# Kernel optimization log

Hardware: AMD Instinct MI355X
Metric: run time of the kernel (lower is better)

Reference implementation:

```python
import jax, jax.numpy as jnp
import numpy as np

B, S, D, H = 4, 2048, 1024, 16
HD = D // H  # head_dim = 64


def setup_inputs() -> dict:
    key = jax.random.key(0)
    ks = jax.random.split(key, 14)
    s = 0.02
    return {
        "inputs_q": jax.random.normal(ks[0], (B, S, D), jnp.float32),
        "pos_emb_q": jax.random.normal(ks[1], (1, S, D), jnp.float32),
        "pos_emb_k": jax.random.normal(ks[2], (1, S, D), jnp.float32),
        "pos_emb_v": jax.random.normal(ks[3], (1, S, D), jnp.float32),
        "attention_bias": jax.random.normal(ks[4], (1, 1, S, S), jnp.float32),
        "attention_bias_kv": jax.random.normal(ks[5], (B, S), jnp.float32),
        "wq": jax.random.normal(ks[6], (D, H, HD), jnp.float32) * s,
        "bq": jnp.zeros((H, HD), jnp.float32),
        "wk": jax.random.normal(ks[7], (D, H, HD), jnp.float32) * s,
        "bk": jnp.zeros((H, HD), jnp.float32),
        "wv": jax.random.normal(ks[8], (D, H, HD), jnp.float32) * s,
        "bv": jnp.zeros((H, HD), jnp.float32),
        "wo": jax.random.normal(ks[9], (H, HD, D), jnp.float32) * s,
        "bo": jnp.zeros((D,), jnp.float32),
    }


def reference(inputs_q, pos_emb_q, pos_emb_k, pos_emb_v, attention_bias,
              attention_bias_kv, wq, bq, wk, bk, wv, bv, wo, bo):
    # Self-attention: inputs_kv = inputs_q. Additive pos-embs BEFORE projection.
    q_in = inputs_q + pos_emb_q
    k_in = inputs_q + pos_emb_k
    v_in = inputs_q + pos_emb_v
    # QKV DenseGeneral: [B,S,D] -> [B,S,H,HD]
    q = jnp.einsum('bsd,dhk->bshk', q_in, wq) + bq
    k = jnp.einsum('bsd,dhk->bshk', k_in, wk) + bk
    v = jnp.einsum('bsd,dhk->bshk', v_in, wv) + bv
    # Scaled dot-product attention with full bias + key-only bias.
    q = q / jnp.sqrt(jnp.asarray(HD, q.dtype))
    scores = jnp.einsum('bqhk,bshk->bhqs', q, k)  # [B,H,Sq,Sk]
    scores = scores + attention_bias + attention_bias_kv[:, None, None, :]
    attn = jax.nn.softmax(scores, axis=-1)
    x = jnp.einsum('bhqs,bshk->bqhk', attn, v)  # [B,S,H,HD]
    # Output projection contracting (H, HD) -> D.
    out = jnp.einsum('bqhk,hkd->bqd', x, wo) + bo
    return out
```

## Files before the change

### kernel.cpp

```cpp
#include <hip/hip_runtime.h>

typedef __attribute__((ext_vector_type(8))) short short8;
typedef __attribute__((ext_vector_type(4))) float f32x4;

#define MFMA16(a, b, c) __builtin_amdgcn_mfma_f32_16x16x32_bf16(a, b, c, 0, 0, 0)

#define SEQ 2048
#define DIM 1024
#define NH 16
#define HD 64
#define LOG2E 1.4426950408889634f

__device__ __forceinline__ ushort f2bf(float f) {
  union { float f; unsigned u; } v; v.f = f;
  unsigned r = (v.u + 0x7FFFu + ((v.u >> 16) & 1u)) >> 16;
  return (ushort)r;
}

__device__ __forceinline__ ushort bf1(float f) {
  unsigned r;
  asm("v_cvt_pk_bf16_f32 %0, %1, %2" : "=v"(r) : "v"(f), "v"(f));
  return (ushort)(r & 0xffffu);
}

__device__ __forceinline__ float exp2fn(float x) {
#if __has_builtin(__builtin_amdgcn_exp2f)
  return __builtin_amdgcn_exp2f(x);
#else
  return exp2f(x);
#endif
}

__global__ __launch_bounds__(256) void prep_a(
    const float* __restrict__ x, const float* __restrict__ pq,
    const float* __restrict__ pk, const float* __restrict__ pv,
    ushort* __restrict__ aq, ushort* __restrict__ ak, ushort* __restrict__ av) {
  int i = (blockIdx.x * 256 + threadIdx.x) * 4;
  int pi = i & (SEQ * DIM - 1);
  float4 xv = *(const float4*)(x + i);
  float4 q4 = *(const float4*)(pq + pi);
  float4 k4 = *(const float4*)(pk + pi);
  float4 v4 = *(const float4*)(pv + pi);
  ushort4 o;
  o.x = f2bf(xv.x + q4.x); o.y = f2bf(xv.y + q4.y);
  o.z = f2bf(xv.z + q4.z); o.w = f2bf(xv.w + q4.w);
  *(ushort4*)(aq + i) = o;
  o.x = f2bf(xv.x + k4.x); o.y = f2bf(xv.y + k4.y);
  o.z = f2bf(xv.z + k4.z); o.w = f2bf(xv.w + k4.w);
  *(ushort4*)(ak + i) = o;
  o.x = f2bf(xv.x + v4.x); o.y = f2bf(xv.y + v4.y);
  o.z = f2bf(xv.z + v4.z); o.w = f2bf(xv.w + v4.w);
  *(ushort4*)(av + i) = o;
}

__global__ __launch_bounds__(256) void transpose_w(
    const float* __restrict__ src, ushort* __restrict__ dst) {
  __shared__ float t[32][33];
  int tx = threadIdx.x & 31, ty = threadIdx.x >> 5;
  int x0 = blockIdx.x * 32, y0 = blockIdx.y * 32;
#pragma unroll
  for (int j = 0; j < 32; j += 8) t[ty + j][tx] = src[(size_t)(y0 + ty + j) * DIM + x0 + tx];
  __syncthreads();
#pragma unroll
  for (int j = 0; j < 32; j += 8)
    dst[(size_t)(x0 + ty + j) * DIM + y0 + tx] = f2bf(t[tx][ty + j]);
}

template <int MODE>
__global__ __launch_bounds__(256) void gemm128(
    const ushort* __restrict__ A, const ushort* __restrict__ Bt,
    const float* __restrict__ bias, void* __restrict__ outp, float scale) {
  constexpr int K = 1024, LDA = 40;
  __shared__ __align__(16) ushort As[128 * LDA];
  __shared__ __align__(16) ushort Bs[128 * LDA];
  const int tid = threadIdx.x;
  const int wave = tid >> 6, lane = tid & 63;
  const int wr = wave >> 1, wc = wave & 1;
  const int g = lane >> 4, l15 = lane & 15;
  const int bm = blockIdx.x, bn = blockIdx.y;
  const int r0 = tid >> 2, c0 = (tid & 3) * 8;
  const ushort* Ap = A + (size_t)(bm * 128 + r0) * K + c0;
  const ushort* Bp = Bt + (size_t)(bn * 128 + r0) * K + c0;
  f32x4 acc[4][4] = {};

  uint4 ra0 = *(const uint4*)(Ap);
  uint4 ra1 = *(const uint4*)(Ap + (size_t)64 * K);
  uint4 rb0 = *(const uint4*)(Bp);
  uint4 rb1 = *(const uint4*)(Bp + (size_t)64 * K);

  for (int kt = 0; kt < K; kt += 32) {
    __syncthreads();
    *(uint4*)&As[r0 * LDA + c0] = ra0;
    *(uint4*)&As[(r0 + 64) * LDA + c0] = ra1;
    *(uint4*)&Bs[r0 * LDA + c0] = rb0;
    *(uint4*)&Bs[(r0 + 64) * LDA + c0] = rb1;
    __syncthreads();
    if (kt + 32 < K) {
      ra0 = *(const uint4*)(Ap + kt + 32);
      ra1 = *(const uint4*)(Ap + (size_t)64 * K + kt + 32);
      rb0 = *(const uint4*)(Bp + kt + 32);
      rb1 = *(const uint4*)(Bp + (size_t)64 * K + kt + 32);
    }
    short8 af[4], bfr[4];
#pragma unroll
    for (int m = 0; m < 4; ++m)
      af[m] = *(const short8*)&As[(wr * 64 + m * 16 + l15) * LDA + g * 8];
#pragma unroll
    for (int n = 0; n < 4; ++n)
      bfr[n] = *(const short8*)&Bs[(wc * 64 + n * 16 + l15) * LDA + g * 8];
#pragma unroll
    for (int m = 0; m < 4; ++m)
#pragma unroll
      for (int n = 0; n < 4; ++n) acc[m][n] = MFMA16(af[m], bfr[n], acc[m][n]);
  }

#pragma unroll
  for (int m = 0; m < 4; ++m) {
    int row = bm * 128 + wr * 64 + m * 16 + g * 4;
#pragma unroll
    for (int n = 0; n < 4; ++n) {
      int col = bn * 128 + wc * 64 + n * 16 + l15;
      float bv = bias[col];
#pragma unroll
      for (int j = 0; j < 4; ++j) {
        float v = (acc[m][n][j] + bv) * scale;
        int r = row + j;
        if (MODE == 0) {
          int b = r >> 11, s = r & (SEQ - 1), h = col >> 6, hd = col & (HD - 1);
          ((ushort*)outp)[((size_t)((b * NH + h) * SEQ + s)) * HD + hd] = f2bf(v);
        } else if (MODE == 2) {
          int b = r >> 11, s = r & (SEQ - 1), h = col >> 6, hd = col & (HD - 1);
          ((ushort*)outp)[((size_t)((b * NH + h) * HD + hd)) * SEQ + s] = f2bf(v);
        } else {
          ((float*)outp)[(size_t)r * DIM + col] = v;
        }
      }
    }
  }
}

__global__ __launch_bounds__(256) void attn5(
    const ushort* __restrict__ Q, const ushort* __restrict__ K,
    const ushort* __restrict__ VT, const float* __restrict__ abias,
    const float* __restrict__ kvbias, ushort* __restrict__ X) {
  constexpr int LDK = 72, LDV = 72, LDP = 72;
  __shared__ __align__(16) ushort Ks[64 * LDK];
  __shared__ __align__(16) ushort Vs[64 * LDV];
  __shared__ __align__(16) ushort Ps[4][32 * LDP];
  const int tid = threadIdx.x;
  const int w = tid >> 6, lane = tid & 63, g = lane >> 4, l15 = lane & 15;
  const int px = blockIdx.x;
  const int qt = (px & 7) | ((px >> 9) << 3);
  const int bh = (px >> 3) & 63;
  const int b = bh >> 4, h = bh & (NH - 1);
  const int q0 = qt * 128;

  short8 qf[2][2];
#pragma unroll
  for (int sub = 0; sub < 2; ++sub) {
    const ushort* qp = Q + ((size_t)bh * SEQ + q0 + w * 32 + sub * 16 + l15) * HD;
#pragma unroll
    for (int c = 0; c < 2; ++c) qf[sub][c] = *(const short8*)(qp + c * 32 + g * 8);
  }

  f32x4 o[2][4] = {};
  float l_lane[2][4] = {};

  const int sr = tid >> 2, scc = (tid & 3) * 16;
  const ushort* Kp = K + (size_t)bh * SEQ * HD;
  const ushort* Vp = VT + (size_t)bh * HD * SEQ;
  const float* abp = abias + (size_t)q0 * SEQ;
  const float* kvp = kvbias + b * SEQ;

  uint4 ka = *(const uint4*)(Kp + (size_t)sr * HD + scc);
  uint4 kb = *(const uint4*)(Kp + (size_t)sr * HD + scc + 8);
  uint4 va = *(const uint4*)(Vp + (size_t)sr * SEQ + scc);
  uint4 vb = *(const uint4*)(Vp + (size_t)sr * SEQ + scc + 8);

  for (int kt = 0; kt < SEQ / 64; ++kt) {
    const int k0 = kt * 64;
    __syncthreads();
    *(uint4*)&Ks[sr * LDK + scc] = ka;
    *(uint4*)&Ks[sr * LDK + scc + 8] = kb;
    *(uint4*)&Vs[sr * LDV + scc] = va;
    *(uint4*)&Vs[sr * LDV + scc + 8] = vb;
    __syncthreads();

    float bkv[4];
#pragma unroll
    for (int ct = 0; ct < 4; ++ct) bkv[ct] = kvp[k0 + ct * 16 + l15];
    float abf[2][4][4];
#pragma unroll
    for (int sub = 0; sub < 2; ++sub)
#pragma unroll
      for (int j = 0; j < 4; ++j) {
        const float* abr = abp + (size_t)(w * 32 + sub * 16 + 4 * g + j) * SEQ + k0 + l15;
#pragma unroll
        for (int ct = 0; ct < 4; ++ct) abf[sub][ct][j] = abr[ct * 16];
      }

    if (kt + 1 < SEQ / 64) {
      ka = *(const uint4*)(Kp + (size_t)(k0 + 64 + sr) * HD + scc);
      kb = *(const uint4*)(Kp + (size_t)(k0 + 64 + sr) * HD + scc + 8);
      va = *(const uint4*)(Vp + (size_t)sr * SEQ + k0 + 64 + scc);
      vb = *(const uint4*)(Vp + (size_t)sr * SEQ + k0 + 64 + scc + 8);
    }

    f32x4 s4[2][4];
#pragma unroll
    for (int ct = 0; ct < 4; ++ct) {
      short8 kf0 = *(const short8*)&Ks[(ct * 16 + l15) * LDK + g * 8];
      short8 kf1 = *(const short8*)&Ks[(ct * 16 + l15) * LDK + 32 + g * 8];
#pragma unroll
      for (int sub = 0; sub < 2; ++sub) {
        f32x4 z = {0.f, 0.f, 0.f, 0.f};
        f32x4 t = MFMA16(qf[sub][0], kf0, z);
        s4[sub][ct] = MFMA16(qf[sub][1], kf1, t);
      }
    }

#pragma unroll
    for (int sub = 0; sub < 2; ++sub) {
      float p[4][4];
#pragma unroll
      for (int ct = 0; ct < 4; ++ct)
#pragma unroll
        for (int j = 0; j < 4; ++j)
          p[ct][j] = exp2fn(fmaf(abf[sub][ct][j] + bkv[ct], LOG2E, s4[sub][ct][j]));
#pragma unroll
      for (int j = 0; j < 4; ++j)
        l_lane[sub][j] += (p[0][j] + p[1][j]) + (p[2][j] + p[3][j]);
#pragma unroll
      for (int ct = 0; ct < 4; ++ct)
#pragma unroll
        for (int j = 0; j < 4; ++j)
          Ps[w][(sub * 16 + 4 * g + j) * LDP + ct * 16 + l15] = bf1(p[ct][j]);
    }

    asm volatile("s_waitcnt lgkmcnt(0)" ::: "memory");
    __builtin_amdgcn_sched_barrier(0);

    short8 pa[2][2];
#pragma unroll
    for (int sub = 0; sub < 2; ++sub)
#pragma unroll
      for (int ks = 0; ks < 2; ++ks)
        pa[sub][ks] = *(const short8*)&Ps[w][(sub * 16 + l15) * LDP + ks * 32 + g * 8];
#pragma unroll
    for (int ctd = 0; ctd < 4; ++ctd) {
      short8 vf0 = *(const short8*)&Vs[(ctd * 16 + l15) * LDV + g * 8];
      short8 vf1 = *(const short8*)&Vs[(ctd * 16 + l15) * LDV + 32 + g * 8];
#pragma unroll
      for (int sub = 0; sub < 2; ++sub) {
        o[sub][ctd] = MFMA16(pa[sub][0], vf0, o[sub][ctd]);
        o[sub][ctd] = MFMA16(pa[sub][1], vf1, o[sub][ctd]);
      }
    }
  }

#pragma unroll
  for (int sub = 0; sub < 2; ++sub) {
    float inv[4];
#pragma unroll
    for (int j = 0; j < 4; ++j) {
      float l = l_lane[sub][j];
      l += __shfl_xor(l, 1);
      l += __shfl_xor(l, 2);
      l += __shfl_xor(l, 4);
      l += __shfl_xor(l, 8);
      inv[j] = 1.0f / l;
    }
#pragma unroll
    for (int ctd = 0; ctd < 4; ++ctd)
#pragma unroll
      for (int j = 0; j < 4; ++j) {
        size_t row = (size_t)b * SEQ + q0 + w * 32 + sub * 16 + 4 * g + j;
        X[row * DIM + h * HD + ctd * 16 + l15] = bf1(o[sub][ctd][j] * inv[j]);
      }
  }
}

extern "C" void kernel_launch(void* const* d_in, const int* in_sizes, int n_in,
                              void* d_out, int out_size, void* d_ws, size_t ws_size,
                              hipStream_t stream) {
  const float* inputs_q = (const float*)d_in[0];
  const float* pos_q = (const float*)d_in[1];
  const float* pos_k = (const float*)d_in[2];
  const float* pos_v = (const float*)d_in[3];
  const float* abias = (const float*)d_in[4];
  const float* kvbias = (const float*)d_in[5];
  const float* wq = (const float*)d_in[6];
  const float* bq = (const float*)d_in[7];
  const float* wk = (const float*)d_in[8];
  const float* bk = (const float*)d_in[9];
  const float* wv = (const float*)d_in[10];
  const float* bv = (const float*)d_in[11];
  const float* wo = (const float*)d_in[12];
  const float* bo = (const float*)d_in[13];

  char* ws = (char*)d_ws;
  const size_t MB = 1ull << 20;
  ushort* wqT = (ushort*)(ws + 0 * MB);
  ushort* wkT = (ushort*)(ws + 2 * MB);
  ushort* wvT = (ushort*)(ws + 4 * MB);
  ushort* woT = (ushort*)(ws + 6 * MB);
  ushort* aq = (ushort*)(ws + 8 * MB);
  ushort* ak = (ushort*)(ws + 24 * MB);
  ushort* av = (ushort*)(ws + 40 * MB);
  ushort* Qb = (ushort*)(ws + 56 * MB);
  ushort* Kb = (ushort*)(ws + 72 * MB);
  ushort* VTb = (ushort*)(ws + 88 * MB);
  ushort* Xb = (ushort*)(ws + 8 * MB);

  prep_a<<<8192, 256, 0, stream>>>(inputs_q, pos_q, pos_k, pos_v, aq, ak, av);
  dim3 tg(32, 32);
  transpose_w<<<tg, 256, 0, stream>>>(wq, wqT);
  transpose_w<<<tg, 256, 0, stream>>>(wk, wkT);
  transpose_w<<<tg, 256, 0, stream>>>(wv, wvT);
  transpose_w<<<tg, 256, 0, stream>>>(wo, woT);
  dim3 gg(64, 8);
  gemm128<0><<<gg, 256, 0, stream>>>(aq, wqT, bq, Qb, 0.125f * LOG2E);
  gemm128<0><<<gg, 256, 0, stream>>>(ak, wkT, bk, Kb, 1.0f);
  gemm128<2><<<gg, 256, 0, stream>>>(av, wvT, bv, VTb, 1.0f);
  attn5<<<1024, 256, 0, stream>>>(Qb, Kb, VTb, abias, kvbias, Xb);
  gemm128<1><<<gg, 256, 0, stream>>>(Xb, woT, bo, d_out, 1.0f);
}
```

Before: 285.1 us.

## Double-buffer K/V shared tiles with XOR swizzle and MFMA priority hints

The attention kernel now keeps two shared-memory buffers for the K and V tiles. The next tile's registers are written into the alternate buffer after the PV MFMAs, which cuts one of the two barriers per iteration. Padding is replaced by an XOR swizzle on 16-byte chunks to avoid LDS bank conflicts, and s_setprio raises wave priority around the MFMA blocks. This doubles K/V LDS usage, which could reduce occupancy, and the swizzle adds index arithmetic.

Result: no change. 289.1 us (+1.4%).

```diff
diff --git a/kernel.cpp b/kernel.cpp
--- a/kernel.cpp
+++ b/kernel.cpp
@@ -139,13 +139,14 @@
   }
 }
 
-__global__ __launch_bounds__(256) void attn5(
+__global__ __launch_bounds__(256) void attn6(
     const ushort* __restrict__ Q, const ushort* __restrict__ K,
     const ushort* __restrict__ VT, const float* __restrict__ abias,
     const float* __restrict__ kvbias, ushort* __restrict__ X) {
-  constexpr int LDK = 72, LDV = 72, LDP = 72;
-  __shared__ __align__(16) ushort Ks[64 * LDK];
-  __shared__ __align__(16) ushort Vs[64 * LDV];
+  constexpr int LDP = 72;
+  constexpr int NT = SEQ / 64;
+  __shared__ __align__(16) ushort Ks[2][64 * 64];
+  __shared__ __align__(16) ushort Vs[2][64 * 64];
   __shared__ __align__(16) ushort Ps[4][32 * LDP];
   const int tid = threadIdx.x;
   const int w = tid >> 6, lane = tid & 63, g = lane >> 4, l15 = lane & 15;
@@ -166,25 +167,32 @@
   f32x4 o[2][4] = {};
   float l_lane[2][4] = {};
 
-  const int sr = tid >> 2, scc = (tid & 3) * 16;
+  const int sr = tid >> 2, sc0 = (tid & 3) * 2;
+  const int wofs0 = sr * 64 + ((sc0 ^ (sr & 7)) * 8);
+  const int wofs1 = sr * 64 + (((sc0 + 1) ^ (sr & 7)) * 8);
+  const int scc = (tid & 3) * 16;
   const ushort* Kp = K + (size_t)bh * SEQ * HD;
   const ushort* Vp = VT + (size_t)bh * HD * SEQ;
   const float* abp = abias + (size_t)q0 * SEQ;
   const float* kvp = kvbias + b * SEQ;
 
+  const int rx = l15 & 7;
+  const int rc0 = (g ^ rx) * 8;
+  const int rc1 = ((4 | g) ^ rx) * 8;
+
   uint4 ka = *(const uint4*)(Kp + (size_t)sr * HD + scc);
   uint4 kb = *(const uint4*)(Kp + (size_t)sr * HD + scc + 8);
   uint4 va = *(const uint4*)(Vp + (size_t)sr * SEQ + scc);
   uint4 vb = *(const uint4*)(Vp + (size_t)sr * SEQ + scc + 8);
-
-  for (int kt = 0; kt < SEQ / 64; ++kt) {
+  *(uint4*)&Ks[0][wofs0] = ka;
+  *(uint4*)&Ks[0][wofs1] = kb;
+  *(uint4*)&Vs[0][wofs0] = va;
+  *(uint4*)&Vs[0][wofs1] = vb;
+  __syncthreads();
+
+  for (int kt = 0; kt < NT; ++kt) {
     const int k0 = kt * 64;
-    __syncthreads();
-    *(uint4*)&Ks[sr * LDK + scc] = ka;
-    *(uint4*)&Ks[sr * LDK + scc + 8] = kb;
-    *(uint4*)&Vs[sr * LDV + scc] = va;
-    *(uint4*)&Vs[sr * LDV + scc + 8] = vb;
-    __syncthreads();
+    const int cur = kt & 1;
 
     float bkv[4];
 #pragma unroll
@@ -199,7 +207,7 @@
         for (int ct = 0; ct < 4; ++ct) abf[sub][ct][j] = abr[ct * 16];
       }
 
-    if (kt + 1 < SEQ / 64) {
+    if (kt + 1 < NT) {
       ka = *(const uint4*)(Kp + (size_t)(k0 + 64 + sr) * HD + scc);
       kb = *(const uint4*)(Kp + (size_t)(k0 + 64 + sr) * HD + scc + 8);
       va = *(const uint4*)(Vp + (size_t)sr * SEQ + k0 + 64 + scc);
@@ -207,10 +215,12 @@
     }
 
     f32x4 s4[2][4];
+    __builtin_amdgcn_s_setprio(1);
 #pragma unroll
     for (int ct = 0; ct < 4; ++ct) {
-      short8 kf0 = *(const short8*)&Ks[(ct * 16 + l15) * LDK + g * 8];
-      short8 kf1 = *(const short8*)&Ks[(ct * 16 + l15) * LDK + 32 + g * 8];
+      const int rk = (ct * 16 + l15) * 64;
+      short8 kf0 = *(const short8*)&Ks[cur][rk + rc0];
+      short8 kf1 = *(const short8*)&Ks[cur][rk + rc1];
 #pragma unroll
       for (int sub = 0; sub < 2; ++sub) {
         f32x4 z = {0.f, 0.f, 0.f, 0.f};
@@ -218,6 +228,7 @@
         s4[sub][ct] = MFMA16(qf[sub][1], kf1, t);
       }
     }
+    __builtin_amdgcn_s_setprio(0);
 
 #pragma unroll
     for (int sub = 0; sub < 2; ++sub) {
@@ -246,15 +257,27 @@
 #pragma unroll
       for (int ks = 0; ks < 2; ++ks)
         pa[sub][ks] = *(const short8*)&Ps[w][(sub * 16 + l15) * LDP + ks * 32 + g * 8];
+    __builtin_amdgcn_s_setprio(1);
 #pragma unroll
     for (int ctd = 0; ctd < 4; ++ctd) {
-      short8 vf0 = *(const short8*)&Vs[(ctd * 16 + l15) * LDV + g * 8];
-      short8 vf1 = *(const short8*)&Vs[(ctd * 16 + l15) * LDV + 32 + g * 8];
+      const int rv = (ctd * 16 + l15) * 64;
+      short8 vf0 = *(const short8*)&Vs[cur][rv + rc0];
+      short8 vf1 = *(const short8*)&Vs[cur][rv + rc1];
 #pragma unroll
       for (int sub = 0; sub < 2; ++sub) {
         o[sub][ctd] = MFMA16(pa[sub][0], vf0, o[sub][ctd]);
         o[sub][ctd] = MFMA16(pa[sub][1], vf1, o[sub][ctd]);
       }
+    }
+    __builtin_amdgcn_s_setprio(0);
+
+    if (kt + 1 < NT) {
+      const int nxt = cur ^ 1;
+      *(uint4*)&Ks[nxt][wofs0] = ka;
+      *(uint4*)&Ks[nxt][wofs1] = kb;
+      *(uint4*)&Vs[nxt][wofs0] = va;
+      *(uint4*)&Vs[nxt][wofs1] = vb;
+      __syncthreads();
     }
   }
 
@@ -322,6 +345,6 @@
   gemm128<0><<<gg, 256, 0, stream>>>(aq, wqT, bq, Qb, 0.125f * LOG2E);
   gemm128<0><<<gg, 256, 0, stream>>>(ak, wkT, bk, Kb, 1.0f);
   gemm128<2><<<gg, 256, 0, stream>>>(av, wvT, bv, VTb, 1.0f);
-  attn5<<<1024, 256, 0, stream>>>(Qb, Kb, VTb, abias, kvbias, Xb);
+  attn6<<<1024, 256, 0, stream>>>(Qb, Kb, VTb, abias, kvbias, Xb);
   gemm128<1><<<gg, 256, 0, stream>>>(Xb, woT, bo, d_out, 1.0f);
 }
```

## Use direct global-to-LDS loads with double-buffered shared tiles in GEMM

Applied to the files above, without the earlier changes.

Replaces the register-staged global loads and LDS stores in the projection GEMM with global_load_lds direct transfers into two ping-pong LDS buffers, cutting one barrier per iteration. The aim is to overlap the next tile's fetch with the current MFMA work and drop the VGPR round-trip. The padding on the LDS rows is removed because the direct loads need a contiguous layout, so fragment reads may now hit bank conflicts. LDS use per block doubles.

Result: slower. 297.0 us (+4.2%).

```diff
diff --git a/kernel.cpp b/kernel.cpp
--- a/kernel.cpp
+++ b/kernel.cpp
@@ -29,6 +29,12 @@
 #else
   return exp2f(x);
 #endif
+}
+
+typedef __attribute__((address_space(3))) unsigned lds_u32_t;
+typedef __attribute__((address_space(1))) const unsigned glob_u32_t;
+__device__ __forceinline__ void gll16(const ushort* g, ushort* l) {
+  __builtin_amdgcn_global_load_lds((glob_u32_t*)g, (lds_u32_t*)l, 16, 0, 0);
 }
 
 __global__ __launch_bounds__(256) void prep_a(
@@ -70,48 +76,53 @@
 __global__ __launch_bounds__(256) void gemm128(
     const ushort* __restrict__ A, const ushort* __restrict__ Bt,
     const float* __restrict__ bias, void* __restrict__ outp, float scale) {
-  constexpr int K = 1024, LDA = 40;
-  __shared__ __align__(16) ushort As[128 * LDA];
-  __shared__ __align__(16) ushort Bs[128 * LDA];
+  constexpr int K = 1024;
+  constexpr int NIT = K / 32;
+  __shared__ __align__(16) ushort As[2][128 * 32];
+  __shared__ __align__(16) ushort Bs[2][128 * 32];
   const int tid = threadIdx.x;
   const int wave = tid >> 6, lane = tid & 63;
   const int wr = wave >> 1, wc = wave & 1;
   const int g = lane >> 4, l15 = lane & 15;
   const int bm = blockIdx.x, bn = blockIdx.y;
-  const int r0 = tid >> 2, c0 = (tid & 3) * 8;
-  const ushort* Ap = A + (size_t)(bm * 128 + r0) * K + c0;
-  const ushort* Bp = Bt + (size_t)(bn * 128 + r0) * K + c0;
+
+  const int c0 = wave * 64 + lane, c1 = c0 + 256;
+  const ushort* gA0 = A + (size_t)(bm * 128 + (c0 >> 2)) * K + (c0 & 3) * 8;
+  const ushort* gA1 = A + (size_t)(bm * 128 + (c1 >> 2)) * K + (c1 & 3) * 8;
+  const ushort* gB0 = Bt + (size_t)(bn * 128 + (c0 >> 2)) * K + (c0 & 3) * 8;
+  const ushort* gB1 = Bt + (size_t)(bn * 128 + (c1 >> 2)) * K + (c1 & 3) * 8;
+  const int lofs0 = wave * 512;
+  const int lofs1 = 2048 + wave * 512;
+
   f32x4 acc[4][4] = {};
 
-  uint4 ra0 = *(const uint4*)(Ap);
-  uint4 ra1 = *(const uint4*)(Ap + (size_t)64 * K);
-  uint4 rb0 = *(const uint4*)(Bp);
-  uint4 rb1 = *(const uint4*)(Bp + (size_t)64 * K);
-
-  for (int kt = 0; kt < K; kt += 32) {
+  gll16(gA0, &As[0][lofs0]);
+  gll16(gA1, &As[0][lofs1]);
+  gll16(gB0, &Bs[0][lofs0]);
+  gll16(gB1, &Bs[0][lofs1]);
+  __syncthreads();
+
+  for (int it = 0; it < NIT; ++it) {
+    const int cur = it & 1, nxt = cur ^ 1;
+    if (it + 1 < NIT) {
+      const int ko = (it + 1) * 32;
+      gll16(gA0 + ko, &As[nxt][lofs0]);
+      gll16(gA1 + ko, &As[nxt][lofs1]);
+      gll16(gB0 + ko, &Bs[nxt][lofs0]);
+      gll16(gB1 + ko, &Bs[nxt][lofs1]);
+    }
+    short8 af[4], bfr[4];
+#pragma unroll
+    for (int m = 0; m < 4; ++m)
+      af[m] = *(const short8*)&As[cur][(wr * 64 + m * 16 + l15) * 32 + g * 8];
+#pragma unroll
+    for (int n = 0; n < 4; ++n)
+      bfr[n] = *(const short8*)&Bs[cur][(wc * 64 + n * 16 + l15) * 32 + g * 8];
+#pragma unroll
+    for (int m = 0; m < 4; ++m)
+#pragma unroll
+      for (int n = 0; n < 4; ++n) acc[m][n] = MFMA16(af[m], bfr[n], acc[m][n]);
     __syncthreads();
-    *(uint4*)&As[r0 * LDA + c0] = ra0;
-    *(uint4*)&As[(r0 + 64) * LDA + c0] = ra1;
-    *(uint4*)&Bs[r0 * LDA + c0] = rb0;
-    *(uint4*)&Bs[(r0 + 64) * LDA + c0] = rb1;
-    __syncthreads();
-    if (kt + 32 < K) {
-      ra0 = *(const uint4*)(Ap + kt + 32);
-      ra1 = *(const uint4*)(Ap + (size_t)64 * K + kt + 32);
-      rb0 = *(const uint4*)(Bp + kt + 32);
-      rb1 = *(const uint4*)(Bp + (size_t)64 * K + kt + 32);
-    }
-    short8 af[4], bfr[4];
-#pragma unroll
-    for (int m = 0; m < 4; ++m)
-      af[m] = *(const short8*)&As[(wr * 64 + m * 16 + l15) * LDA + g * 8];
-#pragma unroll
-    for (int n = 0; n < 4; ++n)
-      bfr[n] = *(const short8*)&Bs[(wc * 64 + n * 16 + l15) * LDA + g * 8];
-#pragma unroll
-    for (int m = 0; m < 4; ++m)
-#pragma unroll
-      for (int n = 0; n < 4; ++n) acc[m][n] = MFMA16(af[m], bfr[n], acc[m][n]);
   }
 
 #pragma unroll
```

## Batch weight transposes and QKV GEMMs, prefetch attention bias one tile ahead

Applied to the files above, without the earlier changes.

Merges the four weight-transpose launches into one 3D-grid launch and the three QKV projection GEMMs into one launch with 1536 blocks, which removes launch overhead and fills the GPU better. The attention kernel now double-buffers the attention-bias and key-bias registers, loading the next tile's bias alongside the K/V prefetch so the global-load latency is hidden behind the current tile's MFMA work. This raises register pressure in the attention kernel, which could lower occupancy.

Result: slower. 356.2 us (+24.9%).

```diff
diff --git a/kernel.cpp b/kernel.cpp
--- a/kernel.cpp
+++ b/kernel.cpp
@@ -53,8 +53,14 @@
   *(ushort4*)(av + i) = o;
 }
 
-__global__ __launch_bounds__(256) void transpose_w(
-    const float* __restrict__ src, ushort* __restrict__ dst) {
+__global__ __launch_bounds__(256) void transpose_all(
+    const float* __restrict__ w0, const float* __restrict__ w1,
+    const float* __restrict__ w2, const float* __restrict__ w3,
+    ushort* __restrict__ d0, ushort* __restrict__ d1,
+    ushort* __restrict__ d2, ushort* __restrict__ d3) {
+  const int z = blockIdx.z;
+  const float* src = z == 0 ? w0 : z == 1 ? w1 : z == 2 ? w2 : w3;
+  ushort* dst = z == 0 ? d0 : z == 1 ? d1 : z == 2 ? d2 : d3;
   __shared__ float t[32][33];
   int tx = threadIdx.x & 31, ty = threadIdx.x >> 5;
   int x0 = blockIdx.x * 32, y0 = blockIdx.y * 32;
@@ -66,10 +72,87 @@
     dst[(size_t)(x0 + ty + j) * DIM + y0 + tx] = f2bf(t[tx][ty + j]);
 }
 
-template <int MODE>
-__global__ __launch_bounds__(256) void gemm128(
+__global__ __launch_bounds__(256) void gemm_qkv(
+    const ushort* __restrict__ aq, const ushort* __restrict__ ak,
+    const ushort* __restrict__ av, const ushort* __restrict__ wqT,
+    const ushort* __restrict__ wkT, const ushort* __restrict__ wvT,
+    const float* __restrict__ bq, const float* __restrict__ bk,
+    const float* __restrict__ bv, ushort* __restrict__ Qb,
+    ushort* __restrict__ Kb, ushort* __restrict__ VTb) {
+  constexpr int K = 1024, LDA = 40;
+  __shared__ __align__(16) ushort As[128 * LDA];
+  __shared__ __align__(16) ushort Bs[128 * LDA];
+  const int proj = blockIdx.y >> 3, bn = blockIdx.y & 7, bm = blockIdx.x;
+  const ushort* A = proj == 0 ? aq : proj == 1 ? ak : av;
+  const ushort* Bt = proj == 0 ? wqT : proj == 1 ? wkT : wvT;
+  const float* bias = proj == 0 ? bq : proj == 1 ? bk : bv;
+  ushort* outp = proj == 0 ? Qb : proj == 1 ? Kb : VTb;
+  const float scale = proj == 0 ? 0.125f * LOG2E : 1.0f;
+
+  const int tid = threadIdx.x;
+  const int wave = tid >> 6, lane = tid & 63;
+  const int wr = wave >> 1, wc = wave & 1;
+  const int g = lane >> 4, l15 = lane & 15;
+  const int r0 = tid >> 2, c0 = (tid & 3) * 8;
+  const ushort* Ap = A + (size_t)(bm * 128 + r0) * K + c0;
+  const ushort* Bp = Bt + (size_t)(bn * 128 + r0) * K + c0;
+  f32x4 acc[4][4] = {};
+
+  uint4 ra0 = *(const uint4*)(Ap);
+  uint4 ra1 = *(const uint4*)(Ap + (size_t)64 * K);
+  uint4 rb0 = *(const uint4*)(Bp);
+  uint4 rb1 = *(const uint4*)(Bp + (size_t)64 * K);
+
+  for (int kt = 0; kt < K; kt += 32) {
+    __syncthreads();
+    *(uint4*)&As[r0 * LDA + c0] = ra0;
+    *(uint4*)&As[(r0 + 64) * LDA + c0] = ra1;
+    *(uint4*)&Bs[r0 * LDA + c0] = rb0;
+    *(uint4*)&Bs[(r0 + 64) * LDA + c0] = rb1;
+    __syncthreads();
+    if (kt + 32 < K) {
+      ra0 = *(const uint4*)(Ap + kt + 32);
+      ra1 = *(const uint4*)(Ap + (size_t)64 * K + kt + 32);
+      rb0 = *(const uint4*)(Bp + kt + 32);
+      rb1 = *(const uint4*)(Bp + (size_t)64 * K + kt + 32);
+    }
+    short8 af[4], bfr[4];
+#pragma unroll
+    for (int m = 0; m < 4; ++m)
+      af[m] = *(const short8*)&As[(wr * 64 + m * 16 + l15) * LDA + g * 8];
+#pragma unroll
+    for (int n = 0; n < 4; ++n)
+      bfr[n] = *(const short8*)&Bs[(wc * 64 + n * 16 + l15) * LDA + g * 8];
+#pragma unroll
+    for (int m = 0; m < 4; ++m)
+#pragma unroll
+      for (int n = 0; n < 4; ++n) acc[m][n] = MFMA16(af[m], bfr[n], acc[m][n]);
+  }
+
+#pragma unroll
+  for (int m = 0; m < 4; ++m) {
+    int row = bm * 128 + wr * 64 + m * 16 + g * 4;
+#pragma unroll
+    for (int n = 0; n < 4; ++n) {
+      int col = bn * 128 + wc * 64 + n * 16 + l15;
+      float bv2 = bias[col];
+#pragma unroll
+      for (int j = 0; j < 4; ++j) {
+        float v = (acc[m][n][j] + bv2) * scale;
+        int r = row + j;
+        int b = r >> 11, s = r & (SEQ - 1), h = col >> 6, hd = col & (HD - 1);
+        if (proj < 2)
+          outp[((size_t)((b * NH + h) * SEQ + s)) * HD + hd] = f2bf(v);
+        else
+          outp[((size_t)((b * NH + h) * HD + hd)) * SEQ + s] = f2bf(v);
+      }
+    }
+  }
+}
+
+__global__ __launch_bounds__(256) void gemm_out(
     const ushort* __restrict__ A, const ushort* __restrict__ Bt,
-    const float* __restrict__ bias, void* __restrict__ outp, float scale) {
+    const float* __restrict__ bias, float* __restrict__ outp) {
   constexpr int K = 1024, LDA = 40;
   __shared__ __align__(16) ushort As[128 * LDA];
   __shared__ __align__(16) ushort Bs[128 * LDA];
@@ -122,28 +205,18 @@
       int col = bn * 128 + wc * 64 + n * 16 + l15;
       float bv = bias[col];
 #pragma unroll
-      for (int j = 0; j < 4; ++j) {
-        float v = (acc[m][n][j] + bv) * scale;
-        int r = row + j;
-        if (MODE == 0) {
-          int b = r >> 11, s = r & (SEQ - 1), h = col >> 6, hd = col & (HD - 1);
-          ((ushort*)outp)[((size_t)((b * NH + h) * SEQ + s)) * HD + hd] = f2bf(v);
-        } else if (MODE == 2) {
-          int b = r >> 11, s = r & (SEQ - 1), h = col >> 6, hd = col & (HD - 1);
-          ((ushort*)outp)[((size_t)((b * NH + h) * HD + hd)) * SEQ + s] = f2bf(v);
-        } else {
-          ((float*)outp)[(size_t)r * DIM + col] = v;
-        }
-      }
-    }
-  }
-}
-
-__global__ __launch_bounds__(256) void attn5(
+      for (int j = 0; j < 4; ++j)
+        outp[(size_t)(row + j) * DIM + col] = acc[m][n][j] + bv;
+    }
+  }
+}
+
+__global__ __launch_bounds__(256) void attn8(
     const ushort* __restrict__ Q, const ushort* __restrict__ K,
     const ushort* __restrict__ VT, const float* __restrict__ abias,
     const float* __restrict__ kvbias, ushort* __restrict__ X) {
   constexpr int LDK = 72, LDV = 72, LDP = 72;
+  constexpr int NT = SEQ / 64;
   __shared__ __align__(16) ushort Ks[64 * LDK];
   __shared__ __align__(16) ushort Vs[64 * LDV];
   __shared__ __align__(16) ushort Ps[4][32 * LDP];
@@ -177,7 +250,27 @@
   uint4 va = *(const uint4*)(Vp + (size_t)sr * SEQ + scc);
   uint4 vb = *(const uint4*)(Vp + (size_t)sr * SEQ + scc + 8);
 
-  for (int kt = 0; kt < SEQ / 64; ++kt) {
+  float bkvA[4], bkvB[4];
+  float abfA[2][4][4], abfB[2][4][4];
+
+  auto loadb = [&](int kt, float (&ab)[2][4][4], float (&kv)[4]) {
+    const int kk = kt * 64;
+#pragma unroll
+    for (int ct = 0; ct < 4; ++ct) kv[ct] = kvp[kk + ct * 16 + l15];
+#pragma unroll
+    for (int sub = 0; sub < 2; ++sub)
+#pragma unroll
+      for (int j = 0; j < 4; ++j) {
+        const float* abr = abp + (size_t)(w * 32 + sub * 16 + 4 * g + j) * SEQ + kk + l15;
+#pragma unroll
+        for (int ct = 0; ct < 4; ++ct) ab[sub][ct][j] = abr[ct * 16];
+      }
+  };
+
+  loadb(0, abfA, bkvA);
+
+  auto tile = [&](int kt, float (&cab)[2][4][4], float (&ckv)[4],
+                  float (&nab)[2][4][4], float (&nkv)[4]) {
     const int k0 = kt * 64;
     __syncthreads();
     *(uint4*)&Ks[sr * LDK + scc] = ka;
@@ -186,20 +279,8 @@
     *(uint4*)&Vs[sr * LDV + scc + 8] = vb;
     __syncthreads();
 
-    float bkv[4];
-#pragma unroll
-    for (int ct = 0; ct < 4; ++ct) bkv[ct] = kvp[k0 + ct * 16 + l15];
-    float abf[2][4][4];
-#pragma unroll
-    for (int sub = 0; sub < 2; ++sub)
-#pragma unroll
-      for (int j = 0; j < 4; ++j) {
-        const float* abr = abp + (size_t)(w * 32 + sub * 16 + 4 * g + j) * SEQ + k0 + l15;
-#pragma unroll
-        for (int ct = 0; ct < 4; ++ct) abf[sub][ct][j] = abr[ct * 16];
-      }
-
-    if (kt + 1 < SEQ / 64) {
+    if (kt + 1 < NT) {
+      loadb(kt + 1, nab, nkv);
       ka = *(const uint4*)(Kp + (size_t)(k0 + 64 + sr) * HD + scc);
       kb = *(const uint4*)(Kp + (size_t)(k0 + 64 + sr) * HD + scc + 8);
       va = *(const uint4*)(Vp + (size_t)sr * SEQ + k0 + 64 + scc);
@@ -226,7 +307,7 @@
       for (int ct = 0; ct < 4; ++ct)
 #pragma unroll
         for (int j = 0; j < 4; ++j)
-          p[ct][j] = exp2fn(fmaf(abf[sub][ct][j] + bkv[ct], LOG2E, s4[sub][ct][j]));
+          p[ct][j] = exp2fn(fmaf(cab[sub][ct][j] + ckv[ct], LOG2E, s4[sub][ct][j]));
 #pragma unroll
       for (int j = 0; j < 4; ++j)
         l_lane[sub][j] += (p[0][j] + p[1][j]) + (p[2][j] + p[3][j]);
@@ -256,6 +337,11 @@
         o[sub][ctd] = MFMA16(pa[sub][1], vf1, o[sub][ctd]);
       }
     }
+  };
+
+  for (int kt = 0; kt < NT; kt += 2) {
+    tile(kt, abfA, bkvA, abfB, bkvB);
+    tile(kt + 1, abfB, bkvB, abfA, bkvA);
   }
 
 #pragma unroll
@@ -313,15 +399,9 @@
   ushort* Xb = (ushort*)(ws + 8 * MB);
 
   prep_a<<<8192, 256, 0, stream>>>(inputs_q, pos_q, pos_k, pos_v, aq, ak, av);
-  dim3 tg(32, 32);
-  transpose_w<<<tg, 256, 0, stream>>>(wq, wqT);
-  transpose_w<<<tg, 256, 0, stream>>>(wk, wkT);
-  transpose_w<<<tg, 256, 0, stream>>>(wv, wvT);
-  transpose_w<<<tg, 256, 0, stream>>>(wo, woT);
-  dim3 gg(64, 8);
-  gemm128<0><<<gg, 256, 0, stream>>>(aq, wqT, bq, Qb, 0.125f * LOG2E);
-  gemm128<0><<<gg, 256, 0, stream>>>(ak, wkT, bk, Kb, 1.0f);
-  gemm128<2><<<gg, 256, 0, stream>>>(av, wvT, bv, VTb, 1.0f);
-  attn5<<<1024, 256, 0, stream>>>(Qb, Kb, VTb, abias, kvbias, Xb);
-  gemm128<1><<<gg, 256, 0, stream>>>(Xb, woT, bo, d_out, 1.0f);
-}
+  transpose_all<<<dim3(32, 32, 4), 256, 0, stream>>>(wq, wk, wv, wo, wqT, wkT, wvT, woT);
+  gemm_qkv<<<dim3(64, 24), 256, 0, stream>>>(aq, ak, av, wqT, wkT, wvT,
+                                             bq, bk, bv, Qb, Kb, VTb);
+  attn8<<<1024, 256, 0, stream>>>(Qb, Kb, VTb, abias, kvbias, Xb);
+  gemm_out<<<dim3(64, 8), 256, 0, stream>>>(Xb, woT, bo, (float*)d_out);
+}
```
